# Kernel optimization log

Measured on AMD Instinct MI355X. Metric: run time of the kernel, lower is better.

Reference implementation:

```python
import jax, jax.numpy as jnp
import numpy as np

B, L, D, K = 64, 200, 256, 8
EPS = 1e-5
SCALE = 1.0 / float(np.sqrt(D))


def _ln(x, g, b):
    mu = jnp.mean(x, -1, keepdims=True)
    var = jnp.mean((x - mu) ** 2, -1, keepdims=True)
    return (x - mu) * jax.lax.rsqrt(var + EPS) * g + b


def setup_inputs() -> dict:
    key = jax.random.key(0)
    ks = jax.random.split(key, 20)
    inp = {
        "local_item_emb": jax.random.normal(ks[0], (B, L, D), jnp.float32),
        "global_item_emb": jax.random.normal(ks[1], (B, L, D), jnp.float32),
        "intentions": jax.random.normal(ks[2], (K, D), jnp.float32),
        "pos_fai": jax.random.normal(ks[3], (L, D), jnp.float32),  # max_len == L here
        "rou": jax.random.normal(ks[4], (D,), jnp.float32),
        "W_w": jax.random.normal(ks[5], (D, D), jnp.float32) * 0.05,
        "W_b": jnp.zeros((D,), jnp.float32),
    }
    for i in range(1, 6):  # 5 LayerNorms, slightly perturbed affines
        inp[f"g{i}"] = 1.0 + 0.1 * jax.random.normal(ks[5 + i], (D,), jnp.float32)
        inp[f"b{i}"] = 0.1 * jax.random.normal(ks[10 + i], (D,), jnp.float32)
    inp["seq_len"] = jax.random.randint(ks[16], (B,), 1, L + 1)  # valid lengths in [1, L]
    return inp


def reference(local_item_emb, global_item_emb, intentions, pos_fai, rou, W_w, W_b,
              g1, b1, g2, b2, g3, b3, g4, b4, g5, b5, seq_len):
    b = local_item_emb.shape[0]

    def disen(item_emb):
        # item -> intention score [B, L, K]
        score = jax.nn.softmax(
            jnp.einsum("bld,kd->blk", _ln(item_emb, g1, b1), _ln(intentions, g2, b2)) * SCALE,
            axis=-1)
        # last-valid-token attention weight [B, L]
        idx = seq_len - 1
        q_row = item_emb[jnp.arange(b), idx] + pos_fai[idx] + rou  # [B, D]
        q = _ln(q_row, g3, b3)
        key_hat = _ln(item_emb + pos_fai[None, :item_emb.shape[1]], g4, b4)
        keyv = key_hat + jax.nn.relu(key_hat @ W_w.T + W_b)
        w = jax.nn.softmax(jnp.einsum("bd,bld->bl", q, keyv) * SCALE, axis=-1)
        # fuse scores and broadcast-multiply into [B, K, L, D]
        fuse = (score * w[..., None]).transpose(0, 2, 1)[..., None]  # [B, K, L, 1]
        return _ln(fuse * item_emb[:, None], g5, b5)

    return disen(local_item_emb) + disen(global_item_emb)
```

## Files before the change

kernel.cpp:

```cpp
#include <hip/hip_runtime.h>

#define Bn 64
#define Ln 200
#define Dn 256
#define Kn 8
#define LPn 224
#define EPSf 1e-5f
#define SCALEf 0.0625f

typedef short bf16x8 __attribute__((ext_vector_type(8)));
typedef float f32x4  __attribute__((ext_vector_type(4)));

__device__ __forceinline__ unsigned short f2bf(float f) {
    unsigned int u = __builtin_bit_cast(unsigned int, f);
    u += 0x7fffu + ((u >> 16) & 1u);
    return (unsigned short)(u >> 16);
}

__device__ __forceinline__ float wsum(float v) {
    v += __shfl_xor(v, 32, 64);
    v += __shfl_xor(v, 16, 64);
    v += __shfl_xor(v, 8, 64);
    v += __shfl_xor(v, 4, 64);
    v += __shfl_xor(v, 2, 64);
    v += __shfl_xor(v, 1, 64);
    return v;
}

__device__ __forceinline__ float gsum16(float v) {
    v += __shfl_xor(v, 1, 64);
    v += __shfl_xor(v, 2, 64);
    v += __shfl_xor(v, 4, 64);
    v += __shfl_xor(v, 8, 64);
    return v;
}

__global__ __launch_bounds__(256) void kprep(
    const float* __restrict__ intentions, const float* __restrict__ g2, const float* __restrict__ b2,
    const float* __restrict__ loc, const float* __restrict__ glob,
    const float* __restrict__ pos, const float* __restrict__ rou,
    const float* __restrict__ g3, const float* __restrict__ b3,
    const int*   __restrict__ seq_len, const float* __restrict__ Ww,
    float* __restrict__ i2hat, float* __restrict__ q, unsigned short* __restrict__ wfrag)
{
    int blk = blockIdx.x, tid = threadIdx.x;
    int lane = tid & 63;
    if (blk < 2) {
        int k = blk * 4 + (tid >> 6);
        const float4 x4 = *(const float4*)(intentions + k * Dn + lane * 4);
        float x[4] = {x4.x, x4.y, x4.z, x4.w};
        float s1 = x[0] + x[1] + x[2] + x[3];
        float s2 = x[0]*x[0] + x[1]*x[1] + x[2]*x[2] + x[3]*x[3];
        s1 = wsum(s1); s2 = wsum(s2);
        float mu = s1 * (1.0f / Dn);
        float var = s2 * (1.0f / Dn) - mu * mu;
        float rs = rsqrtf(var + EPSf);
        const float4 gg = *(const float4*)(g2 + lane * 4);
        const float4 bb = *(const float4*)(b2 + lane * 4);
        float4 o;
        o.x = (x[0]-mu)*rs*gg.x + bb.x; o.y = (x[1]-mu)*rs*gg.y + bb.y;
        o.z = (x[2]-mu)*rs*gg.z + bb.z; o.w = (x[3]-mu)*rs*gg.w + bb.w;
        *(float4*)(i2hat + k * Dn + lane * 4) = o;
    } else if (blk < 34) {
        int wid = (blk - 2) * 4 + (tid >> 6);
        int s = wid / Bn, b = wid % Bn;
        const float* item = s ? glob : loc;
        int idx = seq_len[b] - 1;
        const float4 x4 = *(const float4*)(item + (b * Ln + idx) * Dn + lane * 4);
        const float4 p4 = *(const float4*)(pos + idx * Dn + lane * 4);
        const float4 r4 = *(const float4*)(rou + lane * 4);
        float x[4] = {x4.x + p4.x + r4.x, x4.y + p4.y + r4.y,
                      x4.z + p4.z + r4.z, x4.w + p4.w + r4.w};
        float s1 = x[0] + x[1] + x[2] + x[3];
        float s2 = x[0]*x[0] + x[1]*x[1] + x[2]*x[2] + x[3]*x[3];
        s1 = wsum(s1); s2 = wsum(s2);
        float mu = s1 * (1.0f / Dn);
        float var = s2 * (1.0f / Dn) - mu * mu;
        float rs = rsqrtf(var + EPSf);
        const float4 gg = *(const float4*)(g3 + lane * 4);
        const float4 bb = *(const float4*)(b3 + lane * 4);
        float4 o;
        o.x = (x[0]-mu)*rs*gg.x + bb.x; o.y = (x[1]-mu)*rs*gg.y + bb.y;
        o.z = (x[2]-mu)*rs*gg.z + bb.z; o.w = (x[3]-mu)*rs*gg.w + bb.w;
        *(float4*)(q + wid * Dn + lane * 4) = o;
    } else {
        int gt = (blk - 34) * 256 + tid;
        int frag = gt >> 6, fl = gt & 63;
        int kt = frag >> 4, nt = frag & 15;
        int d = nt * 16 + (fl & 15);
        int e = kt * 32 + (fl >> 4) * 8;
        const float* src = Ww + d * Dn + e;
        unsigned short tmp[8];
#pragma unroll
        for (int j = 0; j < 8; ++j) tmp[j] = f2bf(src[j]);
        ushort4 lo, hi;
        lo.x = tmp[0]; lo.y = tmp[1]; lo.z = tmp[2]; lo.w = tmp[3];
        hi.x = tmp[4]; hi.y = tmp[5]; hi.z = tmp[6]; hi.w = tmp[7];
        unsigned short* dst = wfrag + (size_t)gt * 8;
        *(ushort4*)(dst) = lo;
        *(ushort4*)(dst + 4) = hi;
    }
}

__global__ __launch_bounds__(256) void krow(
    const float* __restrict__ loc, const float* __restrict__ glob, const float* __restrict__ pos,
    const float* __restrict__ g1, const float* __restrict__ b1,
    const float* __restrict__ g4, const float* __restrict__ b4,
    const float* __restrict__ i2hat, const float* __restrict__ q,
    float* __restrict__ score, float* __restrict__ stats, float* __restrict__ qkh,
    unsigned short* __restrict__ kh16)
{
    int gw = blockIdx.x * 4 + (threadIdx.x >> 6);
    int lane = threadIdx.x & 63;
    int grp = lane >> 4, l16 = lane & 15;
    int R = gw * 4 + grp;
    int s = R / (Bn * LPn);
    int rem = R % (Bn * LPn);
    int b = rem / LPn, l = rem % LPn;
    bool valid = l < Ln;
    int lc = valid ? l : 0;
    int doff = l16 * 16;

    const float* item = s ? glob : loc;
    const float* xrow = item + (size_t)(b * Ln + lc) * Dn + doff;
    const float* prow = pos + (size_t)lc * Dn + doff;

    float x[16], p[16];
#pragma unroll
    for (int v = 0; v < 4; ++v) {
        float4 xv = *(const float4*)(xrow + v * 4);
        float4 pv = *(const float4*)(prow + v * 4);
        x[v*4+0] = xv.x; x[v*4+1] = xv.y; x[v*4+2] = xv.z; x[v*4+3] = xv.w;
        p[v*4+0] = pv.x; p[v*4+1] = pv.y; p[v*4+2] = pv.z; p[v*4+3] = pv.w;
    }

    float s1 = 0.f, s2 = 0.f;
#pragma unroll
    for (int i = 0; i < 16; ++i) { s1 += x[i]; s2 = fmaf(x[i], x[i], s2); }
    s1 = gsum16(s1); s2 = gsum16(s2);
    float mu = s1 * (1.0f / Dn);
    float var = s2 * (1.0f / Dn) - mu * mu;
    float rs = rsqrtf(var + EPSf);

    float x1[16];
#pragma unroll
    for (int v = 0; v < 4; ++v) {
        float4 gg = *(const float4*)(g1 + doff + v * 4);
        float4 bb = *(const float4*)(b1 + doff + v * 4);
        x1[v*4+0] = (x[v*4+0]-mu)*rs*gg.x + bb.x;
        x1[v*4+1] = (x[v*4+1]-mu)*rs*gg.y + bb.y;
        x1[v*4+2] = (x[v*4+2]-mu)*rs*gg.z + bb.z;
        x1[v*4+3] = (x[v*4+3]-mu)*rs*gg.w + bb.w;
    }

    float lg[Kn];
#pragma unroll
    for (int k = 0; k < Kn; ++k) {
        const float* iv = i2hat + k * Dn + doff;
        float pk = 0.f;
#pragma unroll
        for (int v = 0; v < 4; ++v) {
            float4 i4 = *(const float4*)(iv + v * 4);
            pk = fmaf(x1[v*4+0], i4.x, pk); pk = fmaf(x1[v*4+1], i4.y, pk);
            pk = fmaf(x1[v*4+2], i4.z, pk); pk = fmaf(x1[v*4+3], i4.w, pk);
        }
        lg[k] = gsum16(pk);
    }
    float mx = -1e30f;
#pragma unroll
    for (int k = 0; k < Kn; ++k) { lg[k] *= SCALEf; mx = fmaxf(mx, lg[k]); }
    float se = 0.f;
    float ex[Kn];
#pragma unroll
    for (int k = 0; k < Kn; ++k) { ex[k] = __expf(lg[k] - mx); se += ex[k]; }
    float inv = 1.0f / se;
    size_t r = (size_t)(s * Bn + b) * Ln + l;
    if (valid) {
        if (l16 < Kn) score[r * Kn + l16] = ex[l16] * inv;
        if (l16 == 0) { float2 st; st.x = mu; st.y = var; *(float2*)(stats + 2 * r) = st; }
    }

    float t1 = 0.f, t2 = 0.f;
    float y[16];
#pragma unroll
    for (int i = 0; i < 16; ++i) { y[i] = x[i] + p[i]; t1 += y[i]; t2 = fmaf(y[i], y[i], t2); }
    t1 = gsum16(t1); t2 = gsum16(t2);
    float muy = t1 * (1.0f / Dn);
    float vay = t2 * (1.0f / Dn) - muy * muy;
    float rsy = rsqrtf(vay + EPSf);
    float kh[16];
#pragma unroll
    for (int v = 0; v < 4; ++v) {
        float4 gg = *(const float4*)(g4 + doff + v * 4);
        float4 bb = *(const float4*)(b4 + doff + v * 4);
        kh[v*4+0] = (y[v*4+0]-muy)*rsy*gg.x + bb.x;
        kh[v*4+1] = (y[v*4+1]-muy)*rsy*gg.y + bb.y;
        kh[v*4+2] = (y[v*4+2]-muy)*rsy*gg.z + bb.z;
        kh[v*4+3] = (y[v*4+3]-muy)*rsy*gg.w + bb.w;
    }
    ushort4 kv[4];
#pragma unroll
    for (int v = 0; v < 4; ++v) {
        kv[v].x = valid ? f2bf(kh[v*4+0]) : (unsigned short)0;
        kv[v].y = valid ? f2bf(kh[v*4+1]) : (unsigned short)0;
        kv[v].z = valid ? f2bf(kh[v*4+2]) : (unsigned short)0;
        kv[v].w = valid ? f2bf(kh[v*4+3]) : (unsigned short)0;
    }
    unsigned short* khrow = kh16 + ((size_t)(s * Bn + b) * LPn + l) * Dn + doff;
    *(ushort4*)(khrow)      = kv[0];
    *(ushort4*)(khrow + 4)  = kv[1];
    *(ushort4*)(khrow + 8)  = kv[2];
    *(ushort4*)(khrow + 12) = kv[3];

    const float* qrow = q + (size_t)(s * Bn + b) * Dn + doff;
    float pq = 0.f;
#pragma unroll
    for (int v = 0; v < 4; ++v) {
        float4 q4 = *(const float4*)(qrow + v * 4);
        pq = fmaf(kh[v*4+0], q4.x, pq); pq = fmaf(kh[v*4+1], q4.y, pq);
        pq = fmaf(kh[v*4+2], q4.z, pq); pq = fmaf(kh[v*4+3], q4.w, pq);
    }
    pq = gsum16(pq);
    if (valid && l16 == 0) qkh[r] = pq;
}

__global__ __launch_bounds__(256) void kgemm(
    const unsigned short* __restrict__ kh16, const unsigned short* __restrict__ wfrag,
    const float* __restrict__ q, const float* __restrict__ Wb,
    const float* __restrict__ qkh, float* __restrict__ wlogit)
{
    int blk = blockIdx.x;
    int sb = blk / 7, mtg = blk % 7;
    int wv = threadIdx.x >> 6, lane = threadIdx.x & 63;

    f32x4 acc[2][4];
#pragma unroll
    for (int mt = 0; mt < 2; ++mt)
#pragma unroll
        for (int nt = 0; nt < 4; ++nt) { acc[mt][nt][0]=0.f; acc[mt][nt][1]=0.f; acc[mt][nt][2]=0.f; acc[mt][nt][3]=0.f; }

    int arow = lane & 15;
    int acol = (lane >> 4) * 8;
    const unsigned short* arowp = kh16 + ((size_t)sb * LPn + mtg * 32 + arow) * Dn + acol;
    const unsigned short* bbase = wfrag + (size_t)(wv * 4) * 64 * 8 + (size_t)lane * 8;

#pragma unroll
    for (int kt = 0; kt < 8; ++kt) {
        bf16x8 af0 = *(const bf16x8*)(arowp + kt * 32);
        bf16x8 af1 = *(const bf16x8*)(arowp + 16 * Dn + kt * 32);
#pragma unroll
        for (int nt = 0; nt < 4; ++nt) {
            bf16x8 bf = *(const bf16x8*)(bbase + ((size_t)(kt * 16 + nt) * 64) * 8);
            acc[0][nt] = __builtin_amdgcn_mfma_f32_16x16x32_bf16(af0, bf, acc[0][nt], 0, 0, 0);
            acc[1][nt] = __builtin_amdgcn_mfma_f32_16x16x32_bf16(af1, bf, acc[1][nt], 0, 0, 0);
        }
    }

    int col = lane & 15, quad = lane >> 4;
    float qv[4], wbv[4];
#pragma unroll
    for (int nt = 0; nt < 4; ++nt) {
        int d = (wv * 4 + nt) * 16 + col;
        qv[nt] = q[(size_t)sb * Dn + d];
        wbv[nt] = Wb[d];
    }
    __shared__ float part[4][32];
#pragma unroll
    for (int mt = 0; mt < 2; ++mt) {
#pragma unroll
        for (int j = 0; j < 4; ++j) {
            float t = 0.f;
#pragma unroll
            for (int nt = 0; nt < 4; ++nt) {
                float v = acc[mt][nt][j] + wbv[nt];
                v = fmaxf(v, 0.f);
                t = fmaf(qv[nt], v, t);
            }
            t += __shfl_xor(t, 1, 64);
            t += __shfl_xor(t, 2, 64);
            t += __shfl_xor(t, 4, 64);
            t += __shfl_xor(t, 8, 64);
            if (col == 0) part[wv][mt * 16 + quad * 4 + j] = t;
        }
    }
    __syncthreads();
    int t = threadIdx.x;
    if (t < 32) {
        int l = mtg * 32 + t;
        if (l < Ln)
            wlogit[(size_t)sb * Ln + l] = qkh[(size_t)sb * Ln + l]
                + part[0][t] + part[1][t] + part[2][t] + part[3][t];
    }
}

__global__ __launch_bounds__(256) void ksoft(const float* __restrict__ wlogit, float* __restrict__ wsoft)
{
    int sb = blockIdx.x, t = threadIdx.x;
    __shared__ float red[4];
    float lg = (t < Ln) ? wlogit[(size_t)sb * Ln + t] * SCALEf : -1e30f;
    float m = lg;
#pragma unroll
    for (int mk = 32; mk >= 1; mk >>= 1) m = fmaxf(m, __shfl_xor(m, mk, 64));
    if ((t & 63) == 0) red[t >> 6] = m;
    __syncthreads();
    m = fmaxf(fmaxf(red[0], red[1]), fmaxf(red[2], red[3]));
    __syncthreads();
    float ex = (t < Ln) ? __expf(lg - m) : 0.f;
    float sm = ex;
#pragma unroll
    for (int mk = 32; mk >= 1; mk >>= 1) sm += __shfl_xor(sm, mk, 64);
    if ((t & 63) == 0) red[t >> 6] = sm;
    __syncthreads();
    sm = red[0] + red[1] + red[2] + red[3];
    if (t < Ln) wsoft[(size_t)sb * Ln + t] = ex / sm;
}

__global__ __launch_bounds__(256) void kout(
    const float* __restrict__ loc, const float* __restrict__ glob,
    const float* __restrict__ score, const float* __restrict__ stats, const float* __restrict__ wsoft,
    const float* __restrict__ g5, const float* __restrict__ b5, float* __restrict__ out)
{
    int rr = threadIdx.x >> 6;
    int lane = threadIdx.x & 63;
    int row = blockIdx.x * 4 + rr;
    int b = row / Ln, l = row % Ln;
    size_t r0 = (size_t)b * Ln + l;
    size_t r1 = (size_t)(Bn + b) * Ln + l;

    float4 x0 = *(const float4*)(loc + (size_t)row * Dn + lane * 4);
    float4 x1 = *(const float4*)(glob + (size_t)row * Dn + lane * 4);
    float2 st0 = *(const float2*)(stats + 2 * r0);
    float2 st1 = *(const float2*)(stats + 2 * r1);
    float w0 = wsoft[r0], w1 = wsoft[r1];
    float4 g5v = *(const float4*)(g5 + lane * 4);
    float4 b5v = *(const float4*)(b5 + lane * 4);

    float4 dx0, dx1;
    dx0.x = x0.x - st0.x; dx0.y = x0.y - st0.x; dx0.z = x0.z - st0.x; dx0.w = x0.w - st0.x;
    dx1.x = x1.x - st1.x; dx1.y = x1.y - st1.x; dx1.z = x1.z - st1.x; dx1.w = x1.w - st1.x;

    float* obase = out + ((size_t)b * Kn * Ln + l) * Dn + lane * 4;
#pragma unroll
    for (int k = 0; k < Kn; ++k) {
        float c0 = score[r0 * Kn + k] * w0;
        float c1 = score[r1 * Kn + k] * w1;
        float a0 = c0 * rsqrtf(fmaf(c0 * c0, st0.y, EPSf));
        float a1 = c1 * rsqrtf(fmaf(c1 * c1, st1.y, EPSf));
        float4 o;
        o.x = fmaf(g5v.x, fmaf(a0, dx0.x, a1 * dx1.x), 2.0f * b5v.x);
        o.y = fmaf(g5v.y, fmaf(a0, dx0.y, a1 * dx1.y), 2.0f * b5v.y);
        o.z = fmaf(g5v.z, fmaf(a0, dx0.z, a1 * dx1.z), 2.0f * b5v.z);
        o.w = fmaf(g5v.w, fmaf(a0, dx0.w, a1 * dx1.w), 2.0f * b5v.w);
        *(float4*)(obase + (size_t)k * Ln * Dn) = o;
    }
}

extern "C" void kernel_launch(void* const* d_in, const int* in_sizes, int n_in,
                              void* d_out, int out_size, void* d_ws, size_t ws_size,
                              hipStream_t stream) {
    const float* loc   = (const float*)d_in[0];
    const float* glob  = (const float*)d_in[1];
    const float* inten = (const float*)d_in[2];
    const float* pos   = (const float*)d_in[3];
    const float* rou   = (const float*)d_in[4];
    const float* Ww    = (const float*)d_in[5];
    const float* Wb    = (const float*)d_in[6];
    const float* g1 = (const float*)d_in[7],  *b1 = (const float*)d_in[8];
    const float* g2 = (const float*)d_in[9],  *b2 = (const float*)d_in[10];
    const float* g3 = (const float*)d_in[11], *b3 = (const float*)d_in[12];
    const float* g4 = (const float*)d_in[13], *b4 = (const float*)d_in[14];
    const float* g5 = (const float*)d_in[15], *b5 = (const float*)d_in[16];
    const int* seq_len = (const int*)d_in[17];
    float* out = (float*)d_out;

    char* ws = (char*)d_ws;
    size_t off = 0;
    float* i2hat = (float*)(ws + off);            off += (size_t)Kn * Dn * 4;
    float* q     = (float*)(ws + off);            off += (size_t)2 * Bn * Dn * 4;
    unsigned short* wfrag = (unsigned short*)(ws + off); off += (size_t)Dn * Dn * 2;
    unsigned short* kh16  = (unsigned short*)(ws + off); off += (size_t)2 * Bn * LPn * Dn * 2;
    float* score  = (float*)(ws + off);           off += (size_t)2 * Bn * Ln * Kn * 4;
    float* stats  = (float*)(ws + off);           off += (size_t)2 * Bn * Ln * 2 * 4;
    float* qkh    = (float*)(ws + off);           off += (size_t)2 * Bn * Ln * 4;
    float* wlogit = (float*)(ws + off);           off += (size_t)2 * Bn * Ln * 4;
    float* wsoft  = (float*)(ws + off);           off += (size_t)2 * Bn * Ln * 4;

    kprep<<<66, 256, 0, stream>>>(inten, g2, b2, loc, glob, pos, rou, g3, b3, seq_len, Ww,
                                  i2hat, q, wfrag);
    krow<<<(2 * Bn * LPn) / 16, 256, 0, stream>>>(loc, glob, pos, g1, b1, g4, b4, i2hat, q,
                                                  score, stats, qkh, kh16);
    kgemm<<<128 * 7, 256, 0, stream>>>(kh16, wfrag, q, Wb, qkh, wlogit);
    ksoft<<<2 * Bn, 256, 0, stream>>>(wlogit, wsoft);
    kout<<<Bn * Ln / 4, 256, 0, stream>>>(loc, glob, score, stats, wsoft, g5, b5, out);
}
```

Measured before the change: 205.9 us.

## Fuse row LayerNorm/score kernel with MFMA key GEMM via shared memory

```diff
diff --git a/kernel.cpp b/kernel.cpp
--- a/kernel.cpp
+++ b/kernel.cpp
@@ -5,6 +5,7 @@
 #define Dn 256
 #define Kn 8
 #define LPn 224
+#define LDSW 264
 #define EPSf 1e-5f
 #define SCALEf 0.0625f
 
@@ -102,136 +103,129 @@
     }
 }
 
-__global__ __launch_bounds__(256) void krow(
+__global__ __launch_bounds__(256) void kfused(
     const float* __restrict__ loc, const float* __restrict__ glob, const float* __restrict__ pos,
     const float* __restrict__ g1, const float* __restrict__ b1,
     const float* __restrict__ g4, const float* __restrict__ b4,
     const float* __restrict__ i2hat, const float* __restrict__ q,
-    float* __restrict__ score, float* __restrict__ stats, float* __restrict__ qkh,
-    unsigned short* __restrict__ kh16)
+    const unsigned short* __restrict__ wfrag, const float* __restrict__ Wb,
+    float* __restrict__ score, float* __restrict__ stats, float* __restrict__ wlogit)
 {
-    int gw = blockIdx.x * 4 + (threadIdx.x >> 6);
-    int lane = threadIdx.x & 63;
+    __shared__ unsigned short khL[32 * LDSW];
+    __shared__ float part[4][32];
+    __shared__ float qkhL[32];
+
+    int sb = blockIdx.x / 7, mtg = blockIdx.x % 7;
+    int s = sb / Bn, b = sb % Bn;
+    int wv = threadIdx.x >> 6, lane = threadIdx.x & 63;
     int grp = lane >> 4, l16 = lane & 15;
-    int R = gw * 4 + grp;
-    int s = R / (Bn * LPn);
-    int rem = R % (Bn * LPn);
-    int b = rem / LPn, l = rem % LPn;
-    bool valid = l < Ln;
-    int lc = valid ? l : 0;
     int doff = l16 * 16;
-
     const float* item = s ? glob : loc;
-    const float* xrow = item + (size_t)(b * Ln + lc) * Dn + doff;
-    const float* prow = pos + (size_t)lc * Dn + doff;
-
-    float x[16], p[16];
-#pragma unroll
-    for (int v = 0; v < 4; ++v) {
-        float4 xv = *(const float4*)(xrow + v * 4);
-        float4 pv = *(const float4*)(prow + v * 4);
-        x[v*4+0] = xv.x; x[v*4+1] = xv.y; x[v*4+2] = xv.z; x[v*4+3] = xv.w;
-        p[v*4+0] = pv.x; p[v*4+1] = pv.y; p[v*4+2] = pv.z; p[v*4+3] = pv.w;
-    }
-
-    float s1 = 0.f, s2 = 0.f;
-#pragma unroll
-    for (int i = 0; i < 16; ++i) { s1 += x[i]; s2 = fmaf(x[i], x[i], s2); }
-    s1 = gsum16(s1); s2 = gsum16(s2);
-    float mu = s1 * (1.0f / Dn);
-    float var = s2 * (1.0f / Dn) - mu * mu;
-    float rs = rsqrtf(var + EPSf);
-
-    float x1[16];
-#pragma unroll
-    for (int v = 0; v < 4; ++v) {
-        float4 gg = *(const float4*)(g1 + doff + v * 4);
-        float4 bb = *(const float4*)(b1 + doff + v * 4);
-        x1[v*4+0] = (x[v*4+0]-mu)*rs*gg.x + bb.x;
-        x1[v*4+1] = (x[v*4+1]-mu)*rs*gg.y + bb.y;
-        x1[v*4+2] = (x[v*4+2]-mu)*rs*gg.z + bb.z;
-        x1[v*4+3] = (x[v*4+3]-mu)*rs*gg.w + bb.w;
-    }
-
-    float lg[Kn];
-#pragma unroll
-    for (int k = 0; k < Kn; ++k) {
-        const float* iv = i2hat + k * Dn + doff;
-        float pk = 0.f;
+
+#pragma unroll
+    for (int it = 0; it < 2; ++it) {
+        int rowL = wv * 8 + it * 4 + grp;
+        int l = mtg * 32 + rowL;
+        bool valid = l < Ln;
+        int lc = valid ? l : 0;
+
+        const float* xrow = item + (size_t)(b * Ln + lc) * Dn + doff;
+        const float* prow = pos + (size_t)lc * Dn + doff;
+        float x[16], p[16];
 #pragma unroll
         for (int v = 0; v < 4; ++v) {
-            float4 i4 = *(const float4*)(iv + v * 4);
-            pk = fmaf(x1[v*4+0], i4.x, pk); pk = fmaf(x1[v*4+1], i4.y, pk);
-            pk = fmaf(x1[v*4+2], i4.z, pk); pk = fmaf(x1[v*4+3], i4.w, pk);
-        }
-        lg[k] = gsum16(pk);
-    }
-    float mx = -1e30f;
-#pragma unroll
-    for (int k = 0; k < Kn; ++k) { lg[k] *= SCALEf; mx = fmaxf(mx, lg[k]); }
-    float se = 0.f;
-    float ex[Kn];
-#pragma unroll
-    for (int k = 0; k < Kn; ++k) { ex[k] = __expf(lg[k] - mx); se += ex[k]; }
-    float inv = 1.0f / se;
-    size_t r = (size_t)(s * Bn + b) * Ln + l;
-    if (valid) {
-        if (l16 < Kn) score[r * Kn + l16] = ex[l16] * inv;
-        if (l16 == 0) { float2 st; st.x = mu; st.y = var; *(float2*)(stats + 2 * r) = st; }
-    }
-
-    float t1 = 0.f, t2 = 0.f;
-    float y[16];
-#pragma unroll
-    for (int i = 0; i < 16; ++i) { y[i] = x[i] + p[i]; t1 += y[i]; t2 = fmaf(y[i], y[i], t2); }
-    t1 = gsum16(t1); t2 = gsum16(t2);
-    float muy = t1 * (1.0f / Dn);
-    float vay = t2 * (1.0f / Dn) - muy * muy;
-    float rsy = rsqrtf(vay + EPSf);
-    float kh[16];
-#pragma unroll
-    for (int v = 0; v < 4; ++v) {
-        float4 gg = *(const float4*)(g4 + doff + v * 4);
-        float4 bb = *(const float4*)(b4 + doff + v * 4);
-        kh[v*4+0] = (y[v*4+0]-muy)*rsy*gg.x + bb.x;
-        kh[v*4+1] = (y[v*4+1]-muy)*rsy*gg.y + bb.y;
-        kh[v*4+2] = (y[v*4+2]-muy)*rsy*gg.z + bb.z;
-        kh[v*4+3] = (y[v*4+3]-muy)*rsy*gg.w + bb.w;
-    }
-    ushort4 kv[4];
-#pragma unroll
-    for (int v = 0; v < 4; ++v) {
-        kv[v].x = valid ? f2bf(kh[v*4+0]) : (unsigned short)0;
-        kv[v].y = valid ? f2bf(kh[v*4+1]) : (unsigned short)0;
-        kv[v].z = valid ? f2bf(kh[v*4+2]) : (unsigned short)0;
-        kv[v].w = valid ? f2bf(kh[v*4+3]) : (unsigned short)0;
-    }
-    unsigned short* khrow = kh16 + ((size_t)(s * Bn + b) * LPn + l) * Dn + doff;
-    *(ushort4*)(khrow)      = kv[0];
-    *(ushort4*)(khrow + 4)  = kv[1];
-    *(ushort4*)(khrow + 8)  = kv[2];
-    *(ushort4*)(khrow + 12) = kv[3];
-
-    const float* qrow = q + (size_t)(s * Bn + b) * Dn + doff;
-    float pq = 0.f;
-#pragma unroll
-    for (int v = 0; v < 4; ++v) {
-        float4 q4 = *(const float4*)(qrow + v * 4);
-        pq = fmaf(kh[v*4+0], q4.x, pq); pq = fmaf(kh[v*4+1], q4.y, pq);
-        pq = fmaf(kh[v*4+2], q4.z, pq); pq = fmaf(kh[v*4+3], q4.w, pq);
-    }
-    pq = gsum16(pq);
-    if (valid && l16 == 0) qkh[r] = pq;
-}
-
-__global__ __launch_bounds__(256) void kgemm(
-    const unsigned short* __restrict__ kh16, const unsigned short* __restrict__ wfrag,
-    const float* __restrict__ q, const float* __restrict__ Wb,
-    const float* __restrict__ qkh, float* __restrict__ wlogit)
-{
-    int blk = blockIdx.x;
-    int sb = blk / 7, mtg = blk % 7;
-    int wv = threadIdx.x >> 6, lane = threadIdx.x & 63;
+            float4 xv = *(const float4*)(xrow + v * 4);
+            float4 pv = *(const float4*)(prow + v * 4);
+            x[v*4+0] = xv.x; x[v*4+1] = xv.y; x[v*4+2] = xv.z; x[v*4+3] = xv.w;
+            p[v*4+0] = pv.x; p[v*4+1] = pv.y; p[v*4+2] = pv.z; p[v*4+3] = pv.w;
+        }
+
+        float s1 = 0.f, s2 = 0.f;
+#pragma unroll
+        for (int i = 0; i < 16; ++i) { s1 += x[i]; s2 = fmaf(x[i], x[i], s2); }
+        s1 = gsum16(s1); s2 = gsum16(s2);
+        float mu = s1 * (1.0f / Dn);
+        float var = s2 * (1.0f / Dn) - mu * mu;
+        float rs = rsqrtf(var + EPSf);
+
+        float x1[16];
+#pragma unroll
+        for (int v = 0; v < 4; ++v) {
+            float4 gg = *(const float4*)(g1 + doff + v * 4);
+            float4 bb = *(const float4*)(b1 + doff + v * 4);
+            x1[v*4+0] = (x[v*4+0]-mu)*rs*gg.x + bb.x;
+            x1[v*4+1] = (x[v*4+1]-mu)*rs*gg.y + bb.y;
+            x1[v*4+2] = (x[v*4+2]-mu)*rs*gg.z + bb.z;
+            x1[v*4+3] = (x[v*4+3]-mu)*rs*gg.w + bb.w;
+        }
+        float lg[Kn];
+#pragma unroll
+        for (int k = 0; k < Kn; ++k) {
+            const float* iv = i2hat + k * Dn + doff;
+            float pk = 0.f;
+#pragma unroll
+            for (int v = 0; v < 4; ++v) {
+                float4 i4 = *(const float4*)(iv + v * 4);
+                pk = fmaf(x1[v*4+0], i4.x, pk); pk = fmaf(x1[v*4+1], i4.y, pk);
+                pk = fmaf(x1[v*4+2], i4.z, pk); pk = fmaf(x1[v*4+3], i4.w, pk);
+            }
+            lg[k] = gsum16(pk);
+        }
+        float mx = -1e30f;
+#pragma unroll
+        for (int k = 0; k < Kn; ++k) { lg[k] *= SCALEf; mx = fmaxf(mx, lg[k]); }
+        float se = 0.f;
+        float ex[Kn];
+#pragma unroll
+        for (int k = 0; k < Kn; ++k) { ex[k] = __expf(lg[k] - mx); se += ex[k]; }
+        float inv = 1.0f / se;
+        size_t r = (size_t)sb * Ln + l;
+        if (valid) {
+            if (l16 < Kn) score[r * Kn + l16] = ex[l16] * inv;
+            if (l16 == 0) { float2 st; st.x = mu; st.y = var; *(float2*)(stats + 2 * r) = st; }
+        }
+
+        float t1 = 0.f, t2 = 0.f;
+        float y[16];
+#pragma unroll
+        for (int i = 0; i < 16; ++i) { y[i] = x[i] + p[i]; t1 += y[i]; t2 = fmaf(y[i], y[i], t2); }
+        t1 = gsum16(t1); t2 = gsum16(t2);
+        float muy = t1 * (1.0f / Dn);
+        float vay = t2 * (1.0f / Dn) - muy * muy;
+        float rsy = rsqrtf(vay + EPSf);
+        float kh[16];
+#pragma unroll
+        for (int v = 0; v < 4; ++v) {
+            float4 gg = *(const float4*)(g4 + doff + v * 4);
+            float4 bb = *(const float4*)(b4 + doff + v * 4);
+            kh[v*4+0] = (y[v*4+0]-muy)*rsy*gg.x + bb.x;
+            kh[v*4+1] = (y[v*4+1]-muy)*rsy*gg.y + bb.y;
+            kh[v*4+2] = (y[v*4+2]-muy)*rsy*gg.z + bb.z;
+            kh[v*4+3] = (y[v*4+3]-muy)*rsy*gg.w + bb.w;
+        }
+        bf16x8 kv0, kv1;
+#pragma unroll
+        for (int j = 0; j < 8; ++j) {
+            kv0[j] = valid ? (short)f2bf(kh[j])     : (short)0;
+            kv1[j] = valid ? (short)f2bf(kh[8 + j]) : (short)0;
+        }
+        unsigned short* dst = khL + rowL * LDSW + doff;
+        *(bf16x8*)(dst)     = kv0;
+        *(bf16x8*)(dst + 8) = kv1;
+
+        const float* qrow = q + (size_t)sb * Dn + doff;
+        float pq = 0.f;
+#pragma unroll
+        for (int v = 0; v < 4; ++v) {
+            float4 q4 = *(const float4*)(qrow + v * 4);
+            pq = fmaf(kh[v*4+0], q4.x, pq); pq = fmaf(kh[v*4+1], q4.y, pq);
+            pq = fmaf(kh[v*4+2], q4.z, pq); pq = fmaf(kh[v*4+3], q4.w, pq);
+        }
+        pq = gsum16(pq);
+        if (l16 == 0) qkhL[rowL] = pq;
+    }
+
+    __syncthreads();
 
     f32x4 acc[2][4];
 #pragma unroll
@@ -241,13 +235,13 @@
 
     int arow = lane & 15;
     int acol = (lane >> 4) * 8;
-    const unsigned short* arowp = kh16 + ((size_t)sb * LPn + mtg * 32 + arow) * Dn + acol;
+    const unsigned short* aL = khL + arow * LDSW + acol;
     const unsigned short* bbase = wfrag + (size_t)(wv * 4) * 64 * 8 + (size_t)lane * 8;
 
 #pragma unroll
     for (int kt = 0; kt < 8; ++kt) {
-        bf16x8 af0 = *(const bf16x8*)(arowp + kt * 32);
-        bf16x8 af1 = *(const bf16x8*)(arowp + 16 * Dn + kt * 32);
+        bf16x8 af0 = *(const bf16x8*)(aL + kt * 32);
+        bf16x8 af1 = *(const bf16x8*)(aL + 16 * LDSW + kt * 32);
 #pragma unroll
         for (int nt = 0; nt < 4; ++nt) {
             bf16x8 bf = *(const bf16x8*)(bbase + ((size_t)(kt * 16 + nt) * 64) * 8);
@@ -264,7 +258,6 @@
         qv[nt] = q[(size_t)sb * Dn + d];
         wbv[nt] = Wb[d];
     }
-    __shared__ float part[4][32];
 #pragma unroll
     for (int mt = 0; mt < 2; ++mt) {
 #pragma unroll
@@ -288,7 +281,7 @@
     if (t < 32) {
         int l = mtg * 32 + t;
         if (l < Ln)
-            wlogit[(size_t)sb * Ln + l] = qkh[(size_t)sb * Ln + l]
+            wlogit[(size_t)sb * Ln + l] = qkhL[t]
                 + part[0][t] + part[1][t] + part[2][t] + part[3][t];
     }
 }
@@ -378,18 +371,15 @@
     float* i2hat = (float*)(ws + off);            off += (size_t)Kn * Dn * 4;
     float* q     = (float*)(ws + off);            off += (size_t)2 * Bn * Dn * 4;
     unsigned short* wfrag = (unsigned short*)(ws + off); off += (size_t)Dn * Dn * 2;
-    unsigned short* kh16  = (unsigned short*)(ws + off); off += (size_t)2 * Bn * LPn * Dn * 2;
     float* score  = (float*)(ws + off);           off += (size_t)2 * Bn * Ln * Kn * 4;
     float* stats  = (float*)(ws + off);           off += (size_t)2 * Bn * Ln * 2 * 4;
-    float* qkh    = (float*)(ws + off);           off += (size_t)2 * Bn * Ln * 4;
     float* wlogit = (float*)(ws + off);           off += (size_t)2 * Bn * Ln * 4;
     float* wsoft  = (float*)(ws + off);           off += (size_t)2 * Bn * Ln * 4;
 
     kprep<<<66, 256, 0, stream>>>(inten, g2, b2, loc, glob, pos, rou, g3, b3, seq_len, Ww,
                                   i2hat, q, wfrag);
-    krow<<<(2 * Bn * LPn) / 16, 256, 0, stream>>>(loc, glob, pos, g1, b1, g4, b4, i2hat, q,
-                                                  score, stats, qkh, kh16);
-    kgemm<<<128 * 7, 256, 0, stream>>>(kh16, wfrag, q, Wb, qkh, wlogit);
+    kfused<<<128 * 7, 256, 0, stream>>>(loc, glob, pos, g1, b1, g4, b4, i2hat, q,
+                                        wfrag, Wb, score, stats, wlogit);
     ksoft<<<2 * Bn, 256, 0, stream>>>(wlogit, wsoft);
     kout<<<Bn * Ln / 4, 256, 0, stream>>>(loc, glob, score, stats, wsoft, g5, b5, out);
 }
```

After: 200.4 us. 2.7% less time.
